# Kernel tuning notes

Hardware: AMD Instinct MI355X
Metric: run time of the kernel (lower is better)

The kernel has to match this reference:

```python
import jax, jax.numpy as jnp
import numpy as np

MAX_PATH_DISTANCE = 5

def setup_inputs() -> dict:
    key = jax.random.key(0)
    k1, k2, k3, k4, k5 = jax.random.split(key, 5)
    N = 8192
    E = 8_000_000
    x = jax.random.normal(k1, (N, 128), dtype=jnp.float32)
    src = jax.random.randint(k2, (E,), 0, N, dtype=jnp.int32)
    dst = jax.random.randint(k3, (E,), 0, N, dtype=jnp.int32)
    # path lengths >= 1 (a path always contains at least the source node)
    path_len = jax.random.randint(k4, (E,), 1, 11, dtype=jnp.int32)
    b = jax.random.normal(k5, (MAX_PATH_DISTANCE,), dtype=jnp.float32)
    return {"x": x, "src": src, "dst": dst, "path_len": path_len, "b": b}

def reference(x, src, dst, path_len, b):
    N = x.shape[0]
    # bias index: min(len, max_path_distance) - 1, clamped to valid range
    idx = jnp.clip(path_len, 1, MAX_PATH_DISTANCE) - 1
    vals = b[idx]                                  # [E] gather from small bias vector
    spatial = jnp.zeros((N, N), dtype=b.dtype)
    spatial = spatial.at[src, dst].set(vals)       # scatter into dense NxN matrix
    return spatial
```

## Files before the change

### kernel.cpp

```cpp
#include <hip/hip_runtime.h>


typedef float floatx4 __attribute__((ext_vector_type(4)));

constexpr int MAXPD      = 5;
constexpr int NROW       = 8192;
constexpr int SLAB_ROWS  = 32;
constexpr int NSLAB      = NROW / SLAB_ROWS;
constexpr int SLOTS_ROW  = NROW / 2;
constexpr int STRIDE     = 9 * SLOTS_ROW;
constexpr int PAIR_CAP   = SLOTS_ROW;
constexpr int CHUNK      = 8192;
constexpr int CUR_PAD    = 16;
constexpr int E_MAX      = 8388606;

__device__ __forceinline__ long long slab_slot(unsigned int s, unsigned int i) {
    unsigned int row = s * 32u + 1u + 2u * (i >> 12);
    return (long long)row * SLOTS_ROW + (i & 4095u);
}

__device__ __forceinline__ float dec(unsigned int k, float b0, float b1,
                                     float b2, float b3, float b4) {
    if (k == 0u) return 0.0f;
    unsigned int bi = k & 7u;
    float v = b0;
    v = (bi == 1u) ? b1 : v;
    v = (bi == 2u) ? b2 : v;
    v = (bi == 3u) ? b3 : v;
    v = (bi == 4u) ? b4 : v;
    return v;
}

__global__ void zero_ws_kernel(unsigned int* __restrict__ w, int n) {
    int i = blockIdx.x * blockDim.x + threadIdx.x;
    if (i < n) w[i] = 0u;
}


__global__ __launch_bounds__(512) void stage1_bin(
        const int* __restrict__ gsrc, const int* __restrict__ gdst,
        const int* __restrict__ gpl, unsigned long long* __restrict__ out64,
        unsigned int* __restrict__ slabcur, int E) {
    __shared__ unsigned long long sorted[CHUNK];
    __shared__ unsigned int hist[NSLAB];
    __shared__ unsigned int offs[NSLAB];
    __shared__ unsigned int cur2[NSLAB];
    __shared__ unsigned int gbase[NSLAB];
    __shared__ unsigned int wsum[4];

    const int t = threadIdx.x;
    const int base = blockIdx.x * CHUNK;
    const int cnt = min(CHUNK, E - base);

    if (t < NSLAB) hist[t] = 0u;
    __syncthreads();

    unsigned long long rec[16];

    #pragma unroll
    for (int k = 0; k < 4; ++k) {
        int g = base + (k * 512 + t) * 4;
        bool full = (g + 3 < E);
        int4 s4 = {0,0,0,0}, d4 = {0,0,0,0}, p4 = {1,1,1,1};
        if (full) {
            s4 = ((const int4*)gsrc)[g >> 2];
            d4 = ((const int4*)gdst)[g >> 2];
            p4 = ((const int4*)gpl)[g >> 2];
        }
        #pragma unroll
        for (int j = 0; j < 4; ++j) {
            int e = g + j;
            unsigned long long r = 0ull;
            if (full || e < E) {
                int ss, dd, pp;
                if (full) {
                    ss = (j == 0) ? s4.x : (j == 1) ? s4.y : (j == 2) ? s4.z : s4.w;
                    dd = (j == 0) ? d4.x : (j == 1) ? d4.y : (j == 2) ? d4.z : d4.w;
                    pp = (j == 0) ? p4.x : (j == 1) ? p4.y : (j == 2) ? p4.z : p4.w;
                } else {
                    ss = gsrc[e]; dd = gdst[e]; pp = gpl[e];
                }
                int bi = pp < 1 ? 0 : (pp > MAXPD ? MAXPD - 1 : pp - 1);
                unsigned int key = (((unsigned int)e + 1u) << 3) | (unsigned int)bi;
                r = ((unsigned long long)key << 26) |
                    ((unsigned long long)(unsigned int)ss << 13) |
                    (unsigned long long)(unsigned int)dd;
                atomicAdd(&hist[(unsigned int)ss >> 5], 1u);
            }
            rec[k * 4 + j] = r;
        }
    }
    __syncthreads();

    unsigned int h = 0, incl = 0;
    if (t < NSLAB) {
        h = hist[t];
        incl = h;
        #pragma unroll
        for (int d = 1; d < 64; d <<= 1) {
            unsigned int v = __shfl_up(incl, d, 64);
            if ((t & 63) >= d) incl += v;
        }
        if ((t & 63) == 63) wsum[t >> 6] = incl;
    }
    __syncthreads();
    if (t < NSLAB) {
        unsigned int wpre = 0;
        for (int w = 0; w < (t >> 6); ++w) wpre += wsum[w];
        unsigned int excl = wpre + incl - h;
        offs[t] = excl;
        cur2[t] = excl;
        gbase[t] = atomicAdd(&slabcur[t * CUR_PAD], h);
    }
    __syncthreads();

    #pragma unroll
    for (int m = 0; m < 16; ++m) {
        unsigned long long r = rec[m];
        if (r) {
            unsigned int slab = (unsigned int)(r >> 18) & 255u;
            unsigned int p = atomicAdd(&cur2[slab], 1u);
            sorted[p] = r;
        }
    }
    __syncthreads();

    for (int i = t; i < cnt; i += 512) {
        unsigned long long r = sorted[i];
        unsigned int slab = (unsigned int)(r >> 18) & 255u;
        unsigned int pos = gbase[slab] + ((unsigned int)i - offs[slab]);
        if (pos < (unsigned int)STRIDE) out64[slab_slot(slab, pos)] = r;
    }
}


__device__ __forceinline__ void s2_process(unsigned long long r,
                                           unsigned int* pcur,
                                           unsigned long long* out64,
                                           unsigned int s) {
    unsigned int q = ((unsigned int)(r >> 14)) & 15u;
    unsigned int pos = atomicAdd(&pcur[q], 1u);
    if (pos < (unsigned int)PAIR_CAP) {
        unsigned int row = s * 32u + 2u * q;
        out64[(long long)row * SLOTS_ROW + pos] = r;
    }
}

__global__ __launch_bounds__(1024) void stage2_rebin(
        unsigned long long* __restrict__ out64,
        const unsigned int* __restrict__ slabcur,
        unsigned int* __restrict__ paircnt) {
    __shared__ unsigned int pcur[16];
    const unsigned int s = blockIdx.x;
    const int t = threadIdx.x;
    if (t < 16) pcur[t] = 0u;
    __syncthreads();
    unsigned int cnt = slabcur[s * CUR_PAD];
    if (cnt > (unsigned int)STRIDE) cnt = STRIDE;
    unsigned int cnt2 = cnt >> 1;
    for (unsigned int i = t; i < cnt2; i += 1024) {
        long long slot = slab_slot(s, 2u * i);
        uint4 v = *reinterpret_cast<const uint4*>(&out64[slot]);
        unsigned long long r0 = ((unsigned long long)v.y << 32) | v.x;
        unsigned long long r1 = ((unsigned long long)v.w << 32) | v.z;
        s2_process(r0, pcur, out64, s);
        s2_process(r1, pcur, out64, s);
    }
    if (t == 0 && (cnt & 1u)) {
        s2_process(out64[slab_slot(s, cnt - 1u)], pcur, out64, s);
    }
    __syncthreads();
    if (t < 16) {
        unsigned int c = pcur[t];
        paircnt[s * 16u + t] = (c > (unsigned int)PAIR_CAP) ? (unsigned int)PAIR_CAP : c;
    }
}


__global__ __launch_bounds__(1024) void stage3_resolve(
        unsigned int* __restrict__ out32,
        const unsigned int* __restrict__ paircnt,
        const float* __restrict__ b) {
    __shared__ unsigned int tab[2 * NROW];
    const int p = blockIdx.x, t = threadIdx.x;
    uint4* t4 = (uint4*)tab;
    #pragma unroll
    for (int j = 0; j < 4; ++j) t4[t + j * 1024] = make_uint4(0u, 0u, 0u, 0u);
    __syncthreads();

    unsigned int cnt = paircnt[p];
    const unsigned long long* list =
        (const unsigned long long*)out32 + (long long)(2 * p) * SLOTS_ROW;
    unsigned int cnt2 = cnt >> 1;
    for (unsigned int i = t; i < cnt2; i += 1024) {
        uint4 v = reinterpret_cast<const uint4*>(list)[i];
        unsigned long long r0 = ((unsigned long long)v.y << 32) | v.x;
        unsigned long long r1 = ((unsigned long long)v.w << 32) | v.z;
        atomicMax(&tab[(((unsigned int)(r0 >> 13)) & 1u) * NROW +
                       ((unsigned int)r0 & 8191u)],
                  (unsigned int)(r0 >> 26));
        atomicMax(&tab[(((unsigned int)(r1 >> 13)) & 1u) * NROW +
                       ((unsigned int)r1 & 8191u)],
                  (unsigned int)(r1 >> 26));
    }
    if (t == 0 && (cnt & 1u)) {
        unsigned long long r = list[cnt - 1u];
        atomicMax(&tab[(((unsigned int)(r >> 13)) & 1u) * NROW +
                       ((unsigned int)r & 8191u)],
                  (unsigned int)(r >> 26));
    }
    __syncthreads();

    const float b0 = b[0], b1 = b[1], b2 = b[2], b3 = b[3], b4 = b[4];
    floatx4* orow = reinterpret_cast<floatx4*>(out32 + (long long)(2 * p) * NROW);
    #pragma unroll
    for (int j = 0; j < 4; ++j) {
        uint4 k = t4[t + j * 1024];
        floatx4 v;
        v.x = dec(k.x, b0, b1, b2, b3, b4);
        v.y = dec(k.y, b0, b1, b2, b3, b4);
        v.z = dec(k.z, b0, b1, b2, b3, b4);
        v.w = dec(k.w, b0, b1, b2, b3, b4);
        __builtin_nontemporal_store(v, &orow[j * 1024 + t]);
    }
}


__global__ void zero_keys_kernel(unsigned int* __restrict__ out, long long n) {
    long long n4 = n >> 2;
    long long i = (long long)blockIdx.x * blockDim.x + threadIdx.x;
    long long stride = (long long)gridDim.x * blockDim.x;
    uint4* p = reinterpret_cast<uint4*>(out);
    for (long long j = i; j < n4; j += stride) p[j] = make_uint4(0u, 0u, 0u, 0u);
    long long base = n4 << 2;
    for (long long j = base + i; j < n; j += stride) out[j] = 0u;
}

__global__ void scatter_keys_kernel(const int* __restrict__ src,
                                    const int* __restrict__ dst,
                                    const int* __restrict__ plen,
                                    unsigned int* __restrict__ keys,
                                    int E, int N) {
    int i = blockIdx.x * blockDim.x + threadIdx.x;
    int stride = gridDim.x * blockDim.x;
    for (int e = i; e < E; e += stride) {
        int s = src[e], d = dst[e], pl = plen[e];
        int bi = pl < 1 ? 0 : (pl > MAXPD ? MAXPD - 1 : pl - 1);
        unsigned int key = (((unsigned int)e + 1u) << 3) | (unsigned int)bi;
        atomicMax(keys + (long long)s * (long long)N + d, key);
    }
}

__global__ void decode_keys_kernel(unsigned int* __restrict__ data, long long n,
                                   const float* __restrict__ b) {
    __shared__ float sb[8];
    if (threadIdx.x < 8) sb[threadIdx.x] = (threadIdx.x < MAXPD) ? b[threadIdx.x] : 0.0f;
    __syncthreads();
    long long n4 = n >> 2;
    long long i = (long long)blockIdx.x * blockDim.x + threadIdx.x;
    long long stride = (long long)gridDim.x * blockDim.x;
    uint4* p = reinterpret_cast<uint4*>(data);
    float4* f = reinterpret_cast<float4*>(data);
    for (long long j = i; j < n4; j += stride) {
        uint4 k = p[j];
        float4 v;
        v.x = k.x ? sb[k.x & 7u] : 0.0f;
        v.y = k.y ? sb[k.y & 7u] : 0.0f;
        v.z = k.z ? sb[k.z & 7u] : 0.0f;
        v.w = k.w ? sb[k.w & 7u] : 0.0f;
        f[j] = v;
    }
    long long base = n4 << 2;
    float* fo = reinterpret_cast<float*>(data);
    for (long long j = base + i; j < n; j += stride) {
        unsigned int k = data[j];
        fo[j] = k ? sb[k & 7u] : 0.0f;
    }
}

extern "C" void kernel_launch(void* const* d_in, const int* in_sizes, int n_in,
                              void* d_out, int out_size, void* d_ws, size_t ws_size,
                              hipStream_t stream) {
    const int* src  = (const int*)d_in[1];
    const int* dst  = (const int*)d_in[2];
    const int* plen = (const int*)d_in[3];
    const float* b  = (const float*)d_in[4];

    int N = in_sizes[0] / 128;
    int E = in_sizes[1];
    long long n = (long long)out_size;

    const size_t ws_need = (size_t)(NSLAB * CUR_PAD + NSLAB * 16) * 4;

    if (N == NROW && n == (long long)NROW * NROW && E > 0 && E <= E_MAX &&
        ws_size >= ws_need) {
        unsigned int* slabcur = (unsigned int*)d_ws;
        unsigned int* paircnt = slabcur + NSLAB * CUR_PAD;
        unsigned long long* out64 = (unsigned long long*)d_out;
        unsigned int* out32 = (unsigned int*)d_out;

        int nzero = NSLAB * CUR_PAD;
        zero_ws_kernel<<<(nzero + 255) / 256, 256, 0, stream>>>(slabcur, nzero);

        int nchunk = (E + CHUNK - 1) / CHUNK;
        stage1_bin<<<nchunk, 512, 0, stream>>>(src, dst, plen, out64, slabcur, E);
        stage2_rebin<<<NSLAB, 1024, 0, stream>>>(out64, slabcur, paircnt);
        stage3_resolve<<<NROW / 2, 1024, 0, stream>>>(out32, paircnt, b);
    } else {
        unsigned int* keys = (unsigned int*)d_out;
        const int BLK = 256;
        int grid_zero = (int)min((n / 4 + BLK - 1) / BLK, (long long)2048);
        int grid_scat = min((E + BLK - 1) / BLK, 2048);
        zero_keys_kernel<<<grid_zero, BLK, 0, stream>>>(keys, n);
        scatter_keys_kernel<<<grid_scat, BLK, 0, stream>>>(src, dst, plen, keys, E, N);
        decode_keys_kernel<<<grid_zero, BLK, 0, stream>>>(keys, n, b);
    }
}
```

Baseline: 142.8 us.

## Use wave-aggregated atomics in rebin, larger bin chunks, nontemporal loads in resolve

Stage 2 now groups records by sub-bin within each 64-lane wavefront using ballots, so one leader lane does a single LDS atomicAdd per bin and the other lanes get their offsets by shuffle and popcount. This replaces one contended atomic per record. Stage 1 doubles the chunk size and block size to 1024 threads, halving the number of blocks and global slab-counter atomics but doubling LDS use per block. Stage 3 reads its record lists with nontemporal loads. The 16-iteration ballot loop adds instruction overhead per record in exchange for less atomic contention.

After: 201.1 us. 40.8% more time.

```diff
diff --git a/kernel.cpp b/kernel.cpp
--- a/kernel.cpp
+++ b/kernel.cpp
@@ -2,6 +2,7 @@
 
 
 typedef float floatx4 __attribute__((ext_vector_type(4)));
+typedef unsigned int uintx4 __attribute__((ext_vector_type(4)));
 
 constexpr int MAXPD      = 5;
 constexpr int NROW       = 8192;
@@ -10,7 +11,7 @@
 constexpr int SLOTS_ROW  = NROW / 2;
 constexpr int STRIDE     = 9 * SLOTS_ROW;
 constexpr int PAIR_CAP   = SLOTS_ROW;
-constexpr int CHUNK      = 8192;
+constexpr int CHUNK      = 16384;
 constexpr int CUR_PAD    = 16;
 constexpr int E_MAX      = 8388606;
 
@@ -37,7 +38,7 @@
 }
 
 
-__global__ __launch_bounds__(512) void stage1_bin(
+__global__ __launch_bounds__(1024) void stage1_bin(
         const int* __restrict__ gsrc, const int* __restrict__ gdst,
         const int* __restrict__ gpl, unsigned long long* __restrict__ out64,
         unsigned int* __restrict__ slabcur, int E) {
@@ -59,7 +60,7 @@
 
     #pragma unroll
     for (int k = 0; k < 4; ++k) {
-        int g = base + (k * 512 + t) * 4;
+        int g = base + (k * 1024 + t) * 4;
         bool full = (g + 3 < E);
         int4 s4 = {0,0,0,0}, d4 = {0,0,0,0}, p4 = {1,1,1,1};
         if (full) {
@@ -125,7 +126,7 @@
     }
     __syncthreads();
 
-    for (int i = t; i < cnt; i += 512) {
+    for (int i = t; i < cnt; i += 1024) {
         unsigned long long r = sorted[i];
         unsigned int slab = (unsigned int)(r >> 18) & 255u;
         unsigned int pos = gbase[slab] + ((unsigned int)i - offs[slab]);
@@ -134,13 +135,25 @@
 }
 
 
-__device__ __forceinline__ void s2_process(unsigned long long r,
-                                           unsigned int* pcur,
-                                           unsigned long long* out64,
-                                           unsigned int s) {
-    unsigned int q = ((unsigned int)(r >> 14)) & 15u;
-    unsigned int pos = atomicAdd(&pcur[q], 1u);
-    if (pos < (unsigned int)PAIR_CAP) {
+__device__ __forceinline__ void s2_process_agg(unsigned long long r, bool valid,
+                                               unsigned int* pcur,
+                                               unsigned long long* out64,
+                                               unsigned int s) {
+    unsigned int q = valid ? (((unsigned int)(r >> 14)) & 15u) : 16u;
+    int lane = threadIdx.x & 63;
+    unsigned int pos = 0xFFFFFFFFu;
+    #pragma unroll
+    for (unsigned int bin = 0; bin < 16; ++bin) {
+        unsigned long long m = __ballot(q == bin);
+        if (q == bin) {
+            int leader = __ffsll((long long)m) - 1;
+            unsigned int base_ = 0;
+            if (lane == leader) base_ = atomicAdd(&pcur[bin], (unsigned int)__popcll(m));
+            base_ = __shfl(base_, leader, 64);
+            pos = base_ + (unsigned int)__popcll(m & ((1ull << lane) - 1ull));
+        }
+    }
+    if (valid && pos < (unsigned int)PAIR_CAP) {
         unsigned int row = s * 32u + 2u * q;
         out64[(long long)row * SLOTS_ROW + pos] = r;
     }
@@ -157,17 +170,23 @@
     __syncthreads();
     unsigned int cnt = slabcur[s * CUR_PAD];
     if (cnt > (unsigned int)STRIDE) cnt = STRIDE;
-    unsigned int cnt2 = cnt >> 1;
-    for (unsigned int i = t; i < cnt2; i += 1024) {
-        long long slot = slab_slot(s, 2u * i);
-        uint4 v = *reinterpret_cast<const uint4*>(&out64[slot]);
-        unsigned long long r0 = ((unsigned long long)v.y << 32) | v.x;
-        unsigned long long r1 = ((unsigned long long)v.w << 32) | v.z;
-        s2_process(r0, pcur, out64, s);
-        s2_process(r1, pcur, out64, s);
-    }
-    if (t == 0 && (cnt & 1u)) {
-        s2_process(out64[slab_slot(s, cnt - 1u)], pcur, out64, s);
+    unsigned int cnt2 = (cnt + 1u) >> 1;
+    unsigned int iters = (cnt2 + 1023u) / 1024u;
+    for (unsigned int it = 0; it < iters; ++it) {
+        unsigned int i = it * 1024u + (unsigned int)t;
+        bool has = (i < cnt2);
+        unsigned long long r0 = 0ull, r1 = 0ull;
+        bool v0 = false, v1 = false;
+        if (has) {
+            long long slot = slab_slot(s, 2u * i);
+            uint4 v = *reinterpret_cast<const uint4*>(&out64[slot]);
+            r0 = ((unsigned long long)v.y << 32) | v.x;
+            r1 = ((unsigned long long)v.w << 32) | v.z;
+            v0 = (2u * i < cnt);
+            v1 = (2u * i + 1u < cnt);
+        }
+        s2_process_agg(r0, v0, pcur, out64, s);
+        s2_process_agg(r1, v1, pcur, out64, s);
     }
     __syncthreads();
     if (t < 16) {
@@ -191,9 +210,10 @@
     unsigned int cnt = paircnt[p];
     const unsigned long long* list =
         (const unsigned long long*)out32 + (long long)(2 * p) * SLOTS_ROW;
+    const uintx4* list4 = reinterpret_cast<const uintx4*>(list);
     unsigned int cnt2 = cnt >> 1;
     for (unsigned int i = t; i < cnt2; i += 1024) {
-        uint4 v = reinterpret_cast<const uint4*>(list)[i];
+        uintx4 v = __builtin_nontemporal_load(&list4[i]);
         unsigned long long r0 = ((unsigned long long)v.y << 32) | v.x;
         unsigned long long r1 = ((unsigned long long)v.w << 32) | v.z;
         atomicMax(&tab[(((unsigned int)(r0 >> 13)) & 1u) * NROW +
@@ -303,7 +323,7 @@
         zero_ws_kernel<<<(nzero + 255) / 256, 256, 0, stream>>>(slabcur, nzero);
 
         int nchunk = (E + CHUNK - 1) / CHUNK;
-        stage1_bin<<<nchunk, 512, 0, stream>>>(src, dst, plen, out64, slabcur, E);
+        stage1_bin<<<nchunk, 1024, 0, stream>>>(src, dst, plen, out64, slabcur, E);
         stage2_rebin<<<NSLAB, 1024, 0, stream>>>(out64, slabcur, paircnt);
         stage3_resolve<<<NROW / 2, 1024, 0, stream>>>(out32, paircnt, b);
     } else {
```
